# Kernel tuning notes

Hardware: AMD Instinct MI355X
Metric: run time of the kernel (lower is better)

## Reference

```python
import jax, jax.numpy as jnp
import numpy as np

EPS = 1e-5


def bn(x, g, b, m, v):
    # eval-mode BatchNorm2d: x [B,C,H,W], params [C]
    s = g / jnp.sqrt(v + EPS)
    return x * s[None, :, None, None] + (b - m * s)[None, :, None, None]


def conv1x1(x, w):
    # x [B,C,H,W], w [O,C]
    return jnp.einsum('bchw,oc->bohw', x, w)


def offset_conv(x, w, b):
    # 3x3 conv, stride 1, pad 1, with bias; x [B,C,H,W], w [18,C,3,3]
    y = jax.lax.conv_general_dilated(x, w, window_strides=(1, 1),
                                     padding=((1, 1), (1, 1)),
                                     dimension_numbers=('NCHW', 'OIHW', 'NCHW'))
    return y + b[None, :, None, None]


def deform_conv3x3(x, offset, w):
    # DeformConv v1: x [B,C,H,W], offset [B,18,H,W] ((dy,dx) pairs per kernel
    # point, torchvision layout), w [O,C,3,3]; stride=1, pad=1, dil=1.
    B, C, H, W = x.shape
    oy = offset[:, 0::2]  # [B,9,H,W]
    ox = offset[:, 1::2]  # [B,9,H,W]
    kgy = (jnp.arange(9) // 3 - 1).astype(x.dtype)  # kernel y offsets
    kgx = (jnp.arange(9) % 3 - 1).astype(x.dtype)   # kernel x offsets
    hh = jnp.arange(H, dtype=x.dtype)
    ww = jnp.arange(W, dtype=x.dtype)
    py = hh[None, None, :, None] + kgy[None, :, None, None] + oy  # [B,9,H,W]
    px = ww[None, None, None, :] + kgx[None, :, None, None] + ox  # [B,9,H,W]
    feat = jnp.transpose(x, (0, 2, 3, 1))  # [B,H,W,C]
    y0 = jnp.floor(py)
    x0 = jnp.floor(px)
    wy = py - y0
    wx = px - x0
    bidx = jnp.arange(B).reshape(B, 1, 1, 1)
    acc = jnp.zeros((B, 9, H, W, C), dtype=x.dtype)
    for dy in (0, 1):
        for dx in (0, 1):
            yi = y0 + dy
            xi = x0 + dx
            wgt = (wy if dy else 1.0 - wy) * (wx if dx else 1.0 - wx)
            valid = (yi >= 0) & (yi <= H - 1) & (xi >= 0) & (xi <= W - 1)
            yic = jnp.clip(yi, 0, H - 1).astype(jnp.int32)
            xic = jnp.clip(xi, 0, W - 1).astype(jnp.int32)
            g = feat[bidx, yic, xic]  # gather -> [B,9,H,W,C]
            acc = acc + (wgt * valid.astype(x.dtype))[..., None] * g
    wk = w.reshape(w.shape[0], C, 9)  # k = ky*3+kx matches kgy/kgx order
    return jnp.einsum('bkhwc,ock->bohw', acc, wk)


def setup_inputs() -> dict:
    key = jax.random.key(0)
    ks = jax.random.split(key, 20)
    B, Cin, H, W = 16, 1024, 32, 32
    P, O = 256, 1024  # width / outplanes
    f32 = jnp.float32
    d = {}
    d['x'] = jax.random.normal(ks[0], (B, Cin, H, W), f32)
    d['w1'] = jax.random.normal(ks[1], (P, Cin), f32) * 0.02
    d['bn1_g'] = 1.0 + 0.1 * jax.random.normal(ks[2], (P,), f32)
    d['bn1_b'] = 0.1 * jax.random.normal(ks[3], (P,), f32)
    d['bn1_m'] = 0.1 * jax.random.normal(ks[4], (P,), f32)
    d['bn1_v'] = 0.5 + jax.random.uniform(ks[5], (P,), f32)
    d['off_w'] = jax.random.normal(ks[6], (18, P, 3, 3), f32) * 0.01
    d['off_b'] = 0.01 * jax.random.normal(ks[7], (18,), f32)
    d['w2'] = jax.random.normal(ks[8], (P, P, 3, 3), f32) * 0.02
    d['bn2_g'] = 1.0 + 0.1 * jax.random.normal(ks[9], (P,), f32)
    d['bn2_b'] = 0.1 * jax.random.normal(ks[10], (P,), f32)
    d['bn2_m'] = 0.1 * jax.random.normal(ks[11], (P,), f32)
    d['bn2_v'] = 0.5 + jax.random.uniform(ks[12], (P,), f32)
    d['w3'] = jax.random.normal(ks[13], (O, P), f32) * 0.02
    d['bn3_g'] = 1.0 + 0.1 * jax.random.normal(ks[14], (O,), f32)
    d['bn3_b'] = 0.1 * jax.random.normal(ks[15], (O,), f32)
    d['bn3_m'] = 0.1 * jax.random.normal(ks[16], (O,), f32)
    d['bn3_v'] = 0.5 + jax.random.uniform(ks[17], (O,), f32)
    return d


def reference(x, w1, bn1_g, bn1_b, bn1_m, bn1_v, off_w, off_b, w2,
              bn2_g, bn2_b, bn2_m, bn2_v, w3, bn3_g, bn3_b, bn3_m, bn3_v):
    shortcut = x
    h = jax.nn.relu(bn(conv1x1(x, w1), bn1_g, bn1_b, bn1_m, bn1_v))
    offset = offset_conv(h, off_w, off_b)
    h = deform_conv3x3(h, offset, w2)
    h = jax.nn.relu(bn(h, bn2_g, bn2_b, bn2_m, bn2_v))
    h = bn(conv1x1(h, w3), bn3_g, bn3_b, bn3_m, bn3_v)
    return jax.nn.relu(h + shortcut)
```

## Files before the change

### kernel.cpp

```cpp
#include <hip/hip_runtime.h>

#define BN_EPS 1e-5f

typedef __bf16 bf16_t;
typedef __bf16 bf16x8 __attribute__((ext_vector_type(8)));
typedef float f32x4 __attribute__((ext_vector_type(4)));


__global__ void __launch_bounds__(1024) k_bnprep(
    const float* g1, const float* b1, const float* m1, const float* v1,
    const float* g2, const float* b2, const float* m2, const float* v2,
    const float* g3, const float* b3, const float* m3, const float* v3,
    float* bnc) {
    int t = threadIdx.x;
    if (t < 256) {
        float s = g1[t] * rsqrtf(v1[t] + BN_EPS);
        bnc[t] = s;
        bnc[256 + t] = b1[t] - m1[t] * s;
        float s2 = g2[t] * rsqrtf(v2[t] + BN_EPS);
        bnc[512 + t] = s2;
        bnc[768 + t] = b2[t] - m2[t] * s2;
    }
    float s3 = g3[t] * rsqrtf(v3[t] + BN_EPS);
    bnc[1024 + t] = s3;
    bnc[2048 + t] = b3[t] - m3[t] * s3;
}

__global__ void __launch_bounds__(256) k_cast(const float* __restrict__ s,
                                              bf16_t* __restrict__ d, int n4) {
    int i = blockIdx.x * 256 + threadIdx.x;
    if (i >= n4) return;
    float4 v = ((const float4*)s)[i];
    d[4 * i + 0] = (bf16_t)v.x;
    d[4 * i + 1] = (bf16_t)v.y;
    d[4 * i + 2] = (bf16_t)v.z;
    d[4 * i + 3] = (bf16_t)v.w;
}

__global__ void __launch_bounds__(256) k_w2f(const float* __restrict__ w2,
                                             bf16_t* __restrict__ w2f) {
    int idx = blockIdx.x * 256 + threadIdx.x;
    if (idx >= 73728) return;
    int lane = idx & 63;
    int rest = idx >> 6;
    int nt = rest & 15;
    int rest2 = rest >> 4;
    int p = rest2 & 7;
    int kp = rest2 >> 3;
    int n = nt * 16 + (lane & 15);
    int c0 = p * 32 + (lane >> 4) * 8;
    bf16x8 r;
#pragma unroll
    for (int e = 0; e < 8; ++e)
        r[e] = (bf16_t)w2[(size_t)n * 2304 + (c0 + e) * 9 + kp];
    *(bf16x8*)(w2f + (size_t)idx * 8) = r;
}

__global__ void __launch_bounds__(256) k_owtb(const float* __restrict__ ow,
                                              bf16_t* __restrict__ owtb) {
    int idx = blockIdx.x * 256 + threadIdx.x;
    if (idx >= 73728) return;
    int j = idx / 2304;
    int rem = idx - j * 2304;
    int kp = rem >> 8;
    int c = rem & 255;
    float v = (j < 18) ? ow[(j * 256 + c) * 9 + kp] : 0.f;
    owtb[idx] = (bf16_t)v;
}

__global__ void __launch_bounds__(256) k_xb(const float* __restrict__ x,
                                            bf16_t* __restrict__ xb) {
    __shared__ float ld[64 * 68];
    int t = threadIdx.x;
    int hw0 = blockIdx.x * 64, c0 = blockIdx.y * 64, b = blockIdx.z;
    int ci = t >> 2, h0 = (t & 3) * 16;
    const float* src = x + ((size_t)(b * 1024 + c0 + ci) << 10) + hw0 + h0;
#pragma unroll
    for (int i = 0; i < 4; ++i)
        *(float4*)(ld + ci * 68 + h0 + 4 * i) = *(const float4*)(src + 4 * i);
    __syncthreads();
    int r = t >> 2, cc0 = (t & 3) * 16;
    bf16x8 o0, o1;
#pragma unroll
    for (int i = 0; i < 8; ++i) o0[i] = (bf16_t)ld[(cc0 + i) * 68 + r];
#pragma unroll
    for (int i = 0; i < 8; ++i) o1[i] = (bf16_t)ld[(cc0 + 8 + i) * 68 + r];
    bf16_t* dst = xb + ((size_t)(b * 1024 + hw0 + r) << 10) + c0 + cc0;
    *(bf16x8*)dst = o0;
    *(bf16x8*)(dst + 8) = o1;
}

__global__ void __launch_bounds__(256) k_gemm64(
    const bf16_t* __restrict__ A, const bf16_t* __restrict__ Bt, int K, int ldo,
    const float* __restrict__ sc, const float* __restrict__ sh,
    const float* __restrict__ resid, bf16_t* __restrict__ outb,
    float* __restrict__ outf, int epi) {
    __shared__ __align__(16) bf16_t As[64 * 40];
    __shared__ __align__(16) bf16_t Bs[128 * 40];
    int t = threadIdx.x;
    int lane = t & 63;
    int w = t >> 6;
    int wm = w >> 1, wn = w & 1;
    int m0 = blockIdx.x * 64, n0 = blockIdx.y * 128;

    int ar = t >> 2, as_ = t & 3;
    const bf16_t* ag = A + (size_t)(m0 + ar) * K + as_ * 8;
    int aw = ar * 40 + ((as_ ^ (ar & 3)) * 8);
    int bn0 = t >> 2, bs_ = t & 3;
    const bf16_t* bg0 = Bt + (size_t)(n0 + bn0) * K + bs_ * 8;
    const bf16_t* bg1 = Bt + (size_t)(n0 + 64 + bn0) * K + bs_ * 8;
    int bw0 = bn0 * 40 + ((bs_ ^ (bn0 & 3)) * 8);
    int bw1 = (64 + bn0) * 40 + ((bs_ ^ (bn0 & 3)) * 8);

    int asel = lane >> 4;
    int ar0 = wm * 32 + (lane & 15);
    int aoff0 = ar0 * 40 + ((asel ^ (ar0 & 3)) * 8);
    int aoff1 = (ar0 + 16) * 40 + ((asel ^ (ar0 & 3)) * 8);
    int boff[4];
#pragma unroll
    for (int ni = 0; ni < 4; ++ni) {
        int n = wn * 64 + ni * 16 + (lane & 15);
        boff[ni] = n * 40 + ((asel ^ (n & 3)) * 8);
    }
    f32x4 acc[2][4] = {};

    for (int k0 = 0; k0 < K; k0 += 32) {
        __syncthreads();
        *(bf16x8*)(As + aw) = *(const bf16x8*)(ag + k0);
        *(bf16x8*)(Bs + bw0) = *(const bf16x8*)(bg0 + k0);
        *(bf16x8*)(Bs + bw1) = *(const bf16x8*)(bg1 + k0);
        __syncthreads();
        bf16x8 a0 = *(const bf16x8*)(As + aoff0);
        bf16x8 a1 = *(const bf16x8*)(As + aoff1);
#pragma unroll
        for (int ni = 0; ni < 4; ++ni) {
            bf16x8 bv = *(const bf16x8*)(Bs + boff[ni]);
            acc[0][ni] = __builtin_amdgcn_mfma_f32_16x16x32_bf16(a0, bv, acc[0][ni], 0, 0, 0);
            acc[1][ni] = __builtin_amdgcn_mfma_f32_16x16x32_bf16(a1, bv, acc[1][ni], 0, 0, 0);
        }
    }

    int mrb = m0 + wm * 32 + (lane >> 4) * 4;
    int ncb = n0 + wn * 64 + (lane & 15);
    if (epi == 0) {
#pragma unroll
        for (int mi = 0; mi < 2; ++mi)
#pragma unroll
            for (int ni = 0; ni < 4; ++ni) {
                int n = ncb + ni * 16;
                float s = sc[n], h = sh[n];
#pragma unroll
                for (int j = 0; j < 4; ++j) {
                    int m = mrb + mi * 16 + j;
                    float v = fmaxf(fmaf(acc[mi][ni][j], s, h), 0.f);
                    outb[(size_t)m * ldo + n] = (bf16_t)v;
                }
            }
    } else {
#pragma unroll
        for (int mi = 0; mi < 2; ++mi) {
            int m = mrb + mi * 16;
            int bb = m >> 10, hw = m & 1023;
#pragma unroll
            for (int ni = 0; ni < 4; ++ni) {
                int o = ncb + ni * 16;
                float s = sc[o], h = sh[o];
                size_t idx = (((size_t)(bb * 1024 + o)) << 10) + hw;
                float4 r = *(const float4*)(resid + idx);
                float4 v;
                v.x = fmaxf(fmaf(acc[mi][ni][0], s, h) + r.x, 0.f);
                v.y = fmaxf(fmaf(acc[mi][ni][1], s, h) + r.y, 0.f);
                v.z = fmaxf(fmaf(acc[mi][ni][2], s, h) + r.z, 0.f);
                v.w = fmaxf(fmaf(acc[mi][ni][3], s, h) + r.w, 0.f);
                *(float4*)(outf + idx) = v;
            }
        }
    }
}

__global__ void __launch_bounds__(256) k_off(const bf16_t* __restrict__ h1,
                                             const bf16_t* __restrict__ owtb,
                                             const float* __restrict__ offb,
                                             float* __restrict__ off) {
    int t = threadIdx.x;
    int lane = t & 63;
    int w = t >> 6;
    int mi = w >> 1, ni = w & 1;
    int y = blockIdx.x, b = blockIdx.y;
    int x = (lane & 15) + mi * 16;
    int ksel = lane >> 4;
    int j = (lane & 15) + ni * 16;
    f32x4 acc = {};
    const bf16_t* h1base = h1 + ((size_t)b << 18);
    const bf16_t* brow = owtb + (size_t)j * 2304 + ksel * 8;

    for (int kp = 0; kp < 9; ++kp) {
        int yy = y + kp / 3 - 1;
        int xx = x + kp % 3 - 1;
        bool vy = (yy >= 0) && (yy < 32);
        bool vx = (xx >= 0) && (xx < 32);
        const bf16_t* arow = h1base + (((size_t)(yy * 32 + xx)) << 8) + ksel * 8;
        const bf16_t* bp = brow + kp * 256;
#pragma unroll
        for (int s = 0; s < 8; ++s) {
            bf16x8 av = {};
            if (vy && vx) av = *(const bf16x8*)(arow + s * 32);
            bf16x8 bv = *(const bf16x8*)(bp + s * 32);
            acc = __builtin_amdgcn_mfma_f32_16x16x32_bf16(av, bv, acc, 0, 0, 0);
        }
    }
    if (j < 18) {
        float bias = offb[j];
        size_t ob = (size_t)b * 18432 + (size_t)j * 1024 + y * 32 + mi * 16;
#pragma unroll
        for (int r = 0; r < 4; ++r) {
            off[ob + ksel * 4 + r] = acc[r] + bias;
        }
    }
}

__global__ void __launch_bounds__(256) k_deform(const bf16_t* __restrict__ h1,
                                                const float* __restrict__ off,
                                                const bf16_t* __restrict__ w2f,
                                                const float* __restrict__ bnc,
                                                bf16_t* __restrict__ h2) {
    __shared__ __align__(16) bf16_t As[2][8 * 1288];
    int t = threadIdx.x;
    int lane = t & 63;
    int wn = t >> 6;
    int y = blockIdx.x, b = blockIdx.y;
    int sx = t >> 3, scg = t & 7;
    int asel = lane >> 4;
    int ar0 = lane & 15;
    int aoff0 = ar0 * 40 + ((asel ^ (ar0 & 3)) * 8);
    int aoff1 = (ar0 + 16) * 40 + ((asel ^ ((ar0 + 16) & 3)) * 8);
    const bf16_t* wfl = w2f + (size_t)(wn * 256 + lane) * 8;
    f32x4 acc[2][4] = {};
    size_t obase = (size_t)b * 18432 + (size_t)y * 32 + sx;
    size_t h1row = (size_t)b * 1024;

    bf16x8 g00[4], g01[4], g10[4], g11[4];
    float w00, w01, w10, w11;

    auto issue_gather = [&](int k) {
        float oy = off[obase + (size_t)(2 * k) * 1024];
        float ox = off[obase + (size_t)(2 * k + 1) * 1024];
        float py = (float)y + (float)(k / 3 - 1) + oy;
        float px = (float)sx + (float)(k % 3 - 1) + ox;
        float fy = floorf(py), fx = floorf(px);
        float wy = py - fy, wx = px - fx;
        int y0 = (int)fy, x0 = (int)fx;
        int y1 = y0 + 1, x1 = x0 + 1;
        float vy0 = (y0 >= 0 && y0 < 32) ? 1.f : 0.f;
        float vy1 = (y1 >= 0 && y1 < 32) ? 1.f : 0.f;
        float vx0 = (x0 >= 0 && x0 < 32) ? 1.f : 0.f;
        float vx1 = (x1 >= 0 && x1 < 32) ? 1.f : 0.f;
        int yc0 = min(max(y0, 0), 31), yc1 = min(max(y1, 0), 31);
        int xc0 = min(max(x0, 0), 31), xc1 = min(max(x1, 0), 31);
        w00 = (1.f - wy) * (1.f - wx) * vy0 * vx0;
        w01 = (1.f - wy) * wx * vy0 * vx1;
        w10 = wy * (1.f - wx) * vy1 * vx0;
        w11 = wy * wx * vy1 * vx1;
        const bf16_t* p00 = h1 + ((h1row + yc0 * 32 + xc0) << 8);
        const bf16_t* p01 = h1 + ((h1row + yc0 * 32 + xc1) << 8);
        const bf16_t* p10 = h1 + ((h1row + yc1 * 32 + xc0) << 8);
        const bf16_t* p11 = h1 + ((h1row + yc1 * 32 + xc1) << 8);
#pragma unroll
        for (int q = 0; q < 4; ++q) {
            int c = scg * 32 + q * 8;
            g00[q] = *(const bf16x8*)(p00 + c);
            g01[q] = *(const bf16x8*)(p01 + c);
            g10[q] = *(const bf16x8*)(p10 + c);
            g11[q] = *(const bf16x8*)(p11 + c);
        }
    };
    auto cvt_write = [&](int buf) {
        bf16_t* pnl = &As[buf][scg * 1288 + sx * 40];
#pragma unroll
        for (int q = 0; q < 4; ++q) {
            bf16x8 r;
#pragma unroll
            for (int e = 0; e < 8; ++e) {
                float f = w00 * (float)g00[q][e] + w01 * (float)g01[q][e] +
                          w10 * (float)g10[q][e] + w11 * (float)g11[q][e];
                r[e] = (bf16_t)f;
            }
            *(bf16x8*)(pnl + ((q ^ (sx & 3)) * 8)) = r;
        }
    };

    issue_gather(0);
    cvt_write(0);
    __syncthreads();

    for (int k = 0; k < 9; ++k) {
        int cur = k & 1;
        if (k < 8) issue_gather(k + 1);
        const bf16_t* wfk = wfl + (size_t)k * 65536;
        bf16x8 bb[2][4];
#pragma unroll
        for (int ni = 0; ni < 4; ++ni)
            bb[0][ni] = *(const bf16x8*)(wfk + ni * 512);
#pragma unroll
        for (int ni = 0; ni < 4; ++ni)
            bb[1][ni] = *(const bf16x8*)(wfk + 8192 + ni * 512);
#pragma unroll
        for (int p = 0; p < 4; ++p) {
            const bf16_t* pb = &As[cur][p * 1288];
            bf16x8 a0 = *(const bf16x8*)(pb + aoff0);
            bf16x8 a1 = *(const bf16x8*)(pb + aoff1);
#pragma unroll
            for (int ni = 0; ni < 4; ++ni) {
                bf16x8 bv = bb[p & 1][ni];
                acc[0][ni] = __builtin_amdgcn_mfma_f32_16x16x32_bf16(a0, bv, acc[0][ni], 0, 0, 0);
                acc[1][ni] = __builtin_amdgcn_mfma_f32_16x16x32_bf16(a1, bv, acc[1][ni], 0, 0, 0);
            }
#pragma unroll
            for (int ni = 0; ni < 4; ++ni)
                bb[p & 1][ni] = *(const bf16x8*)(wfk + (p + 2) * 8192 + ni * 512);
        }
        if (k < 8) cvt_write(cur ^ 1);
#pragma unroll
        for (int p = 4; p < 8; ++p) {
            const bf16_t* pb = &As[cur][p * 1288];
            bf16x8 a0 = *(const bf16x8*)(pb + aoff0);
            bf16x8 a1 = *(const bf16x8*)(pb + aoff1);
#pragma unroll
            for (int ni = 0; ni < 4; ++ni) {
                bf16x8 bv = bb[p & 1][ni];
                acc[0][ni] = __builtin_amdgcn_mfma_f32_16x16x32_bf16(a0, bv, acc[0][ni], 0, 0, 0);
                acc[1][ni] = __builtin_amdgcn_mfma_f32_16x16x32_bf16(a1, bv, acc[1][ni], 0, 0, 0);
            }
            if (p + 2 < 8) {
#pragma unroll
                for (int ni = 0; ni < 4; ++ni)
                    bb[p & 1][ni] = *(const bf16x8*)(wfk + (p + 2) * 8192 + ni * 512);
            }
        }
        __syncthreads();
    }
    int mrb = (lane >> 4) * 4;
    int ncb = wn * 64 + (lane & 15);
#pragma unroll
    for (int mi = 0; mi < 2; ++mi)
#pragma unroll
        for (int ni = 0; ni < 4; ++ni) {
            int n = ncb + ni * 16;
            float s = bnc[512 + n], h = bnc[768 + n];
#pragma unroll
            for (int j = 0; j < 4; ++j) {
                int row = mrb + mi * 16 + j;
                float v = fmaxf(fmaf(acc[mi][ni][j], s, h), 0.f);
                h2[(((size_t)(b * 1024 + y * 32 + row)) << 8) + n] = (bf16_t)v;
            }
        }
}

extern "C" void kernel_launch(void* const* d_in, const int* in_sizes, int n_in,
                              void* d_out, int out_size, void* d_ws, size_t ws_size,
                              hipStream_t stream) {
    const float* x = (const float*)d_in[0];
    const float* w1 = (const float*)d_in[1];
    const float* bn1g = (const float*)d_in[2];
    const float* bn1b = (const float*)d_in[3];
    const float* bn1m = (const float*)d_in[4];
    const float* bn1v = (const float*)d_in[5];
    const float* off_w = (const float*)d_in[6];
    const float* off_b = (const float*)d_in[7];
    const float* w2 = (const float*)d_in[8];
    const float* bn2g = (const float*)d_in[9];
    const float* bn2b = (const float*)d_in[10];
    const float* bn2m = (const float*)d_in[11];
    const float* bn2v = (const float*)d_in[12];
    const float* w3 = (const float*)d_in[13];
    const float* bn3g = (const float*)d_in[14];
    const float* bn3b = (const float*)d_in[15];
    const float* bn3m = (const float*)d_in[16];
    const float* bn3v = (const float*)d_in[17];
    float* out = (float*)d_out;

    char* ws = (char*)d_ws;
    float* bnc = (float*)(ws + 0);
    bf16_t* owtb = (bf16_t*)(ws + 12288);
    float* off = (float*)(ws + 178176);
    bf16_t* xb = (bf16_t*)(ws + 1357824);
    bf16_t* w1b = (bf16_t*)(ws + 34912256);
    bf16_t* w2fb = (bf16_t*)(ws + 35436544);
    bf16_t* w3b = (bf16_t*)(ws + 36616192);
    bf16_t* h1b = (bf16_t*)(ws + 37140480);
    bf16_t* h2b = (bf16_t*)(ws + 45529088);

    k_bnprep<<<1, 1024, 0, stream>>>(bn1g, bn1b, bn1m, bn1v, bn2g, bn2b, bn2m,
                                     bn2v, bn3g, bn3b, bn3m, bn3v, bnc);
    k_cast<<<256, 256, 0, stream>>>(w1, w1b, 65536);
    k_cast<<<256, 256, 0, stream>>>(w3, w3b, 65536);
    k_w2f<<<288, 256, 0, stream>>>(w2, w2fb);
    k_owtb<<<288, 256, 0, stream>>>(off_w, owtb);
    k_xb<<<dim3(16, 16, 16), 256, 0, stream>>>(x, xb);
    k_gemm64<<<dim3(256, 2), 256, 0, stream>>>(xb, w1b, 1024, 256, bnc,
                                               bnc + 256, nullptr, h1b, nullptr, 0);
    k_off<<<dim3(32, 16), 256, 0, stream>>>(h1b, owtb, off_b, off);
    k_deform<<<dim3(32, 16), 256, 0, stream>>>(h1b, off, w2fb, bnc, h2b);
    k_gemm64<<<dim3(256, 8), 256, 0, stream>>>(h2b, w3b, 256, 1024, bnc + 1024,
                                               bnc + 2048, x, nullptr, out, 1);
}
```

Baseline: 294.3 us.

## Double-buffer GEMM LDS tiles and fuse offset conv into deform kernel

The GEMM main loop now uses two LDS buffers and prefetches the next K-tile into registers while MFMAs run on the current tile, which halves the barriers per iteration. Separately, the standalone offset-conv kernel is removed. Each deform block computes its own row's 18 offset channels with MFMA into shared memory before gathering. This drops one launch and the global offset round trip, at the cost of doubled LDS in the GEMM and extra serial work at the start of each deform block.

```diff
diff --git a/kernel.cpp b/kernel.cpp
--- a/kernel.cpp
+++ b/kernel.cpp
@@ -95,8 +95,8 @@
     const float* __restrict__ sc, const float* __restrict__ sh,
     const float* __restrict__ resid, bf16_t* __restrict__ outb,
     float* __restrict__ outf, int epi) {
-    __shared__ __align__(16) bf16_t As[64 * 40];
-    __shared__ __align__(16) bf16_t Bs[128 * 40];
+    __shared__ __align__(16) bf16_t As[2][64 * 40];
+    __shared__ __align__(16) bf16_t Bs[2][128 * 40];
     int t = threadIdx.x;
     int lane = t & 63;
     int w = t >> 6;
@@ -124,20 +124,36 @@
     }
     f32x4 acc[2][4] = {};
 
-    for (int k0 = 0; k0 < K; k0 += 32) {
-        __syncthreads();
-        *(bf16x8*)(As + aw) = *(const bf16x8*)(ag + k0);
-        *(bf16x8*)(Bs + bw0) = *(const bf16x8*)(bg0 + k0);
-        *(bf16x8*)(Bs + bw1) = *(const bf16x8*)(bg1 + k0);
-        __syncthreads();
-        bf16x8 a0 = *(const bf16x8*)(As + aoff0);
-        bf16x8 a1 = *(const bf16x8*)(As + aoff1);
+    bf16x8 ra = *(const bf16x8*)(ag);
+    bf16x8 rb0 = *(const bf16x8*)(bg0);
+    bf16x8 rb1 = *(const bf16x8*)(bg1);
+    *(bf16x8*)(As[0] + aw) = ra;
+    *(bf16x8*)(Bs[0] + bw0) = rb0;
+    *(bf16x8*)(Bs[0] + bw1) = rb1;
+    __syncthreads();
+
+    int nt = K >> 5;
+    for (int ti = 0; ti < nt; ++ti) {
+        int cur = ti & 1;
+        if (ti + 1 < nt) {
+            ra = *(const bf16x8*)(ag + (ti + 1) * 32);
+            rb0 = *(const bf16x8*)(bg0 + (ti + 1) * 32);
+            rb1 = *(const bf16x8*)(bg1 + (ti + 1) * 32);
+        }
+        bf16x8 a0 = *(const bf16x8*)(As[cur] + aoff0);
+        bf16x8 a1 = *(const bf16x8*)(As[cur] + aoff1);
 #pragma unroll
         for (int ni = 0; ni < 4; ++ni) {
-            bf16x8 bv = *(const bf16x8*)(Bs + boff[ni]);
+            bf16x8 bv = *(const bf16x8*)(Bs[cur] + boff[ni]);
             acc[0][ni] = __builtin_amdgcn_mfma_f32_16x16x32_bf16(a0, bv, acc[0][ni], 0, 0, 0);
             acc[1][ni] = __builtin_amdgcn_mfma_f32_16x16x32_bf16(a1, bv, acc[1][ni], 0, 0, 0);
         }
+        if (ti + 1 < nt) {
+            *(bf16x8*)(As[cur ^ 1] + aw) = ra;
+            *(bf16x8*)(Bs[cur ^ 1] + bw0) = rb0;
+            *(bf16x8*)(Bs[cur ^ 1] + bw1) = rb1;
+        }
+        __syncthreads();
     }
 
     int mrb = m0 + wm * 32 + (lane >> 4) * 4;
@@ -178,53 +194,14 @@
     }
 }
 
-__global__ void __launch_bounds__(256) k_off(const bf16_t* __restrict__ h1,
-                                             const bf16_t* __restrict__ owtb,
-                                             const float* __restrict__ offb,
-                                             float* __restrict__ off) {
-    int t = threadIdx.x;
-    int lane = t & 63;
-    int w = t >> 6;
-    int mi = w >> 1, ni = w & 1;
-    int y = blockIdx.x, b = blockIdx.y;
-    int x = (lane & 15) + mi * 16;
-    int ksel = lane >> 4;
-    int j = (lane & 15) + ni * 16;
-    f32x4 acc = {};
-    const bf16_t* h1base = h1 + ((size_t)b << 18);
-    const bf16_t* brow = owtb + (size_t)j * 2304 + ksel * 8;
-
-    for (int kp = 0; kp < 9; ++kp) {
-        int yy = y + kp / 3 - 1;
-        int xx = x + kp % 3 - 1;
-        bool vy = (yy >= 0) && (yy < 32);
-        bool vx = (xx >= 0) && (xx < 32);
-        const bf16_t* arow = h1base + (((size_t)(yy * 32 + xx)) << 8) + ksel * 8;
-        const bf16_t* bp = brow + kp * 256;
-#pragma unroll
-        for (int s = 0; s < 8; ++s) {
-            bf16x8 av = {};
-            if (vy && vx) av = *(const bf16x8*)(arow + s * 32);
-            bf16x8 bv = *(const bf16x8*)(bp + s * 32);
-            acc = __builtin_amdgcn_mfma_f32_16x16x32_bf16(av, bv, acc, 0, 0, 0);
-        }
-    }
-    if (j < 18) {
-        float bias = offb[j];
-        size_t ob = (size_t)b * 18432 + (size_t)j * 1024 + y * 32 + mi * 16;
-#pragma unroll
-        for (int r = 0; r < 4; ++r) {
-            off[ob + ksel * 4 + r] = acc[r] + bias;
-        }
-    }
-}
-
 __global__ void __launch_bounds__(256) k_deform(const bf16_t* __restrict__ h1,
-                                                const float* __restrict__ off,
+                                                const bf16_t* __restrict__ owtb,
+                                                const float* __restrict__ offb,
                                                 const bf16_t* __restrict__ w2f,
                                                 const float* __restrict__ bnc,
                                                 bf16_t* __restrict__ h2) {
     __shared__ __align__(16) bf16_t As[2][8 * 1288];
+    __shared__ float offs[18 * 33];
     int t = threadIdx.x;
     int lane = t & 63;
     int wn = t >> 6;
@@ -236,15 +213,44 @@
     int aoff1 = (ar0 + 16) * 40 + ((asel ^ ((ar0 + 16) & 3)) * 8);
     const bf16_t* wfl = w2f + (size_t)(wn * 256 + lane) * 8;
     f32x4 acc[2][4] = {};
-    size_t obase = (size_t)b * 18432 + (size_t)y * 32 + sx;
     size_t h1row = (size_t)b * 1024;
+
+    {
+        int mi = wn >> 1, ni = wn & 1;
+        int xq = (lane & 15) + mi * 16;
+        int ks2 = lane >> 4;
+        int jq = (lane & 15) + ni * 16;
+        f32x4 oacc = {};
+        const bf16_t* browq = owtb + (size_t)jq * 2304 + ks2 * 8;
+        for (int kp = 0; kp < 9; ++kp) {
+            int yy = y + kp / 3 - 1;
+            int xx = xq + kp % 3 - 1;
+            bool vv = (yy >= 0) && (yy < 32) && (xx >= 0) && (xx < 32);
+            const bf16_t* arow = h1 + ((h1row + yy * 32 + xx) << 8) + ks2 * 8;
+            const bf16_t* bp = browq + kp * 256;
+#pragma unroll
+            for (int s = 0; s < 8; ++s) {
+                bf16x8 av = {};
+                if (vv) av = *(const bf16x8*)(arow + s * 32);
+                bf16x8 bv = *(const bf16x8*)(bp + s * 32);
+                oacc = __builtin_amdgcn_mfma_f32_16x16x32_bf16(av, bv, oacc, 0, 0, 0);
+            }
+        }
+        if (jq < 18) {
+            float bias = offb[jq];
+#pragma unroll
+            for (int r = 0; r < 4; ++r)
+                offs[jq * 33 + mi * 16 + ks2 * 4 + r] = oacc[r] + bias;
+        }
+    }
+    __syncthreads();
 
     bf16x8 g00[4], g01[4], g10[4], g11[4];
     float w00, w01, w10, w11;
 
     auto issue_gather = [&](int k) {
-        float oy = off[obase + (size_t)(2 * k) * 1024];
-        float ox = off[obase + (size_t)(2 * k + 1) * 1024];
+        float oy = offs[(2 * k) * 33 + sx];
+        float ox = offs[(2 * k + 1) * 33 + sx];
         float py = (float)y + (float)(k / 3 - 1) + oy;
         float px = (float)sx + (float)(k % 3 - 1) + ox;
         float fy = floorf(py), fx = floorf(px);
@@ -382,7 +388,6 @@
     char* ws = (char*)d_ws;
     float* bnc = (float*)(ws + 0);
     bf16_t* owtb = (bf16_t*)(ws + 12288);
-    float* off = (float*)(ws + 178176);
     bf16_t* xb = (bf16_t*)(ws + 1357824);
     bf16_t* w1b = (bf16_t*)(ws + 34912256);
     bf16_t* w2fb = (bf16_t*)(ws + 35436544);
@@ -399,8 +404,7 @@
     k_xb<<<dim3(16, 16, 16), 256, 0, stream>>>(x, xb);
     k_gemm64<<<dim3(256, 2), 256, 0, stream>>>(xb, w1b, 1024, 256, bnc,
                                                bnc + 256, nullptr, h1b, nullptr, 0);
-    k_off<<<dim3(32, 16), 256, 0, stream>>>(h1b, owtb, off_b, off);
-    k_deform<<<dim3(32, 16), 256, 0, stream>>>(h1b, off, w2fb, bnc, h2b);
+    k_deform<<<dim3(32, 16), 256, 0, stream>>>(h1b, owtb, off_b, w2fb, bnc, h2b);
     k_gemm64<<<dim3(256, 8), 256, 0, stream>>>(h2b, w3b, 256, 1024, bnc + 1024,
                                                bnc + 2048, x, nullptr, out, 1);
 }
```

After: 288.1 us. 1.02x faster.
